# Kernel tuning notes

Measured on AMD Instinct MI355X. Metric: run time of the kernel, lower is better.

Reference implementation:

```python
import jax, jax.numpy as jnp
import numpy as np

B, N = 2, 131072          # batch, expanded node slots (divisible by flag_size)
FEAT = 69                 # org(3) + pos(3) + uids(63)
KERNELS = 128
FLAG_SIZE = 4             # 1 << dims, dims = 2
BINS = 16                 # 1 << flag_size


def _conv1d(x, w, b, stride=1, padding='SAME'):
    # keras Conv1D: x [B,N,Cin], w [K,Cin,Cout], relu activation
    y = jax.lax.conv_general_dilated(x, w, (stride,), padding,
                                     dimension_numbers=('NWC', 'WIO', 'NWC'))
    return jax.nn.relu(y + b)


def setup_inputs() -> dict:
    key = jax.random.key(0)
    ks = jax.random.split(key, 12)

    def g(k, shape):
        fan_in = int(np.prod(shape[:-1]))
        return (jax.random.normal(k, shape, jnp.float32) / np.sqrt(fan_in)).astype(jnp.float32)

    c_x = FEAT + KERNELS                 # 197 after each pre conv concat
    c_flags = 2 * FEAT + KERNELS         # 266 flags-head input
    c_sym = c_flags + FLAG_SIZE          # 270 symbols-branch input

    return {
        'inputs': jax.random.normal(ks[0], (B, N, FEAT), jnp.float32),
        'w_pre0': g(ks[1], (3, FEAT, KERNELS)),   'b_pre0': jnp.zeros((KERNELS,), jnp.float32),
        'w_pre1': g(ks[2], (3, c_x, KERNELS)),    'b_pre1': jnp.zeros((KERNELS,), jnp.float32),
        'w_flags': g(ks[3], (c_flags, FLAG_SIZE)), 'b_flags': jnp.zeros((FLAG_SIZE,), jnp.float32),
        'w_merge': g(ks[4], (FLAG_SIZE, c_sym, KERNELS)), 'b_merge': jnp.zeros((KERNELS,), jnp.float32),
        'w_post0': g(ks[5], (3, KERNELS, KERNELS)), 'b_post0': jnp.zeros((KERNELS,), jnp.float32),
        'w_post1': g(ks[6], (3, KERNELS, KERNELS)), 'b_post1': jnp.zeros((KERNELS,), jnp.float32),
        'w_post2': g(ks[7], (3, KERNELS, KERNELS)), 'b_post2': jnp.zeros((KERNELS,), jnp.float32),
        'w_post3': g(ks[8], (3, KERNELS, KERNELS)), 'b_post3': jnp.zeros((KERNELS,), jnp.float32),
        'w_sym': g(ks[9], (KERNELS, BINS)),        'b_sym': jnp.zeros((BINS,), jnp.float32),
    }


def _forward(inputs, w_pre0, b_pre0, w_pre1, b_pre1, w_flags, b_flags,
             w_merge, b_merge, w_post0, b_post0, w_post1, b_post1,
             w_post2, b_post2, w_post3, b_post3, w_sym, b_sym):
    # pos offsets = (3, 6); pos = inputs[..., 3:5] (2 columns)
    pos = inputs[..., 3:5]
    sort = jnp.argsort(pos, axis=-2)                       # [B, N, 2]
    # gather with batch_dims=1 along node axis
    X = jnp.take_along_axis(inputs, sort[..., 1:2], axis=1)   # sorted by pos col 1
    x0 = jax.lax.stop_gradient(X)                            # [B, N, 69]
    X = jnp.concatenate([x0, _conv1d(X, w_pre0, b_pre0)], axis=-1)  # [B, N, 197]
    X = jnp.concatenate([x0, _conv1d(X, w_pre1, b_pre1)], axis=-1)  # [B, N, 197]
    X = jnp.concatenate([X, jnp.take_along_axis(inputs, sort[..., 0:1], axis=1)], axis=-1)  # [B, N, 266]

    F = jax.nn.sigmoid(X @ w_flags + b_flags)               # [B, N, 4]

    S = jax.lax.stop_gradient(jnp.concatenate([F, X], axis=-1))     # [B, N, 270]
    S = _conv1d(S, w_merge, b_merge, stride=FLAG_SIZE, padding='VALID')  # [B, N/4, 128]
    for w, b in ((w_post0, b_post0), (w_post1, b_post1), (w_post2, b_post2), (w_post3, b_post3)):
        S = _conv1d(S, w, b)
    S = jax.nn.softmax(S @ w_sym + b_sym, axis=-1)          # [B, N/4, 16]

    Fd = (F[..., 0] - F[..., 1]).reshape(F.shape[0], -1, FLAG_SIZE)  # [B, N/4, 4]
    return jnp.concatenate([Fd, S], axis=-1)                # [B, N/4, 20]


def reference(inputs, w_pre0, b_pre0, w_pre1, b_pre1, w_flags, b_flags,
              w_merge, b_merge, w_post0, b_post0, w_post1, b_post1,
              w_post2, b_post2, w_post3, b_post3, w_sym, b_sym):
    return _forward(inputs, w_pre0, b_pre0, w_pre1, b_pre1, w_flags, b_flags,
                    w_merge, b_merge, w_post0, b_post0, w_post1, b_post1,
                    w_post2, b_post2, w_post3, b_post3, w_sym, b_sym)
```

## Files before the change

### kernel.cpp

```cpp
#include <hip/hip_runtime.h>
#include <hip/hip_bf16.h>
#include <math.h>

#define NPOS 131072
#define NF   69
#define NMRG 32768
#define TILE 2048
#define TPS  64
#define NSORT 4
#define EPT  16
#define XCW  288

typedef __attribute__((ext_vector_type(8))) short short8;
typedef __attribute__((ext_vector_type(4))) short s16x4;
typedef __bf16 bf16x8 __attribute__((ext_vector_type(8)));
typedef __attribute__((ext_vector_type(4))) float f32x4;

static __device__ inline bf16x8 as_bf16x8(short8 v){ union{short8 s; bf16x8 b;} u; u.s=v; return u.b; }
static __device__ inline short f2bf(float x){ __hip_bfloat16 h = __float2bfloat16(x); return *(short*)&h; }
static __device__ inline float bf2f(short s){ return __uint_as_float(((unsigned)(unsigned short)s)<<16); }

static __device__ inline void gld16(const short* g, short* l){
  __builtin_amdgcn_global_load_lds(
      (const __attribute__((address_space(1))) unsigned int*)g,
      (__attribute__((address_space(3))) unsigned int*)l, 16, 0, 0);
}

__global__ void k_make_keys(const float* __restrict__ inp, unsigned* __restrict__ kA,
                            unsigned* __restrict__ vA){
  unsigned t = blockIdx.x*256u + threadIdx.x;
  unsigned s = t >> 17, i = t & (NPOS-1u);
  unsigned b = s >> 1, ch = 3u + (s & 1u);
  float x = inp[((size_t)b*NPOS + i)*NF + ch];
  unsigned u = __float_as_uint(x);
  u = (u & 0x80000000u) ? ~u : (u | 0x80000000u);
  kA[t] = u; vA[t] = i;
}

__global__ __launch_bounds__(256) void k_hist(const unsigned* __restrict__ src,
                                              unsigned* __restrict__ hist, int shift){
  __shared__ unsigned h[256];
  int tid = threadIdx.x;
  h[tid] = 0u; __syncthreads();
  int s = blockIdx.x / TPS, tile = blockIdx.x % TPS;
  const unsigned* ks = src + (size_t)s*NPOS + (size_t)tile*TILE;
  for (int r = 0; r < TILE/256; ++r){
    unsigned d = (ks[r*256 + tid] >> shift) & 255u;
    atomicAdd(&h[d], 1u);
  }
  __syncthreads();
  hist[s*16384 + tid*TPS + tile] = h[tid];
}

__global__ __launch_bounds__(256) void k_scan(unsigned* __restrict__ hist){
  __shared__ unsigned tot[256];
  int tid = threadIdx.x; int s = blockIdx.x;
  unsigned* g = hist + s*16384;
  unsigned sum = 0;
  for (int q = 0; q < TPS; ++q) sum += g[tid*TPS + q];
  tot[tid] = sum;
  __syncthreads();
  if (tid == 0){
    unsigned run = 0;
    for (int t = 0; t < 256; ++t){ unsigned tmp = tot[t]; tot[t] = run; run += tmp; }
  }
  __syncthreads();
  unsigned run = tot[tid];
  for (int q = 0; q < TPS; ++q){ unsigned tmp = g[tid*TPS+q]; g[tid*TPS+q] = run; run += tmp; }
}

__global__ __launch_bounds__(128) void k_scatter(const unsigned* __restrict__ srcK,
    const unsigned* __restrict__ srcV, unsigned* __restrict__ dstK, unsigned* __restrict__ dstV,
    const unsigned* __restrict__ off, int shift){
  __shared__ unsigned short cnt[256*128];
  int tid = threadIdx.x;
  unsigned* cz = (unsigned*)cnt;
  for (int idx = tid; idx < 256*128/2; idx += 128) cz[idx] = 0u;
  __syncthreads();
  int s = blockIdx.x / TPS, tile = blockIdx.x % TPS;
  const unsigned* ks = srcK + (size_t)s*NPOS + (size_t)tile*TILE;
  const unsigned* vs = srcV + (size_t)s*NPOS + (size_t)tile*TILE;
  unsigned k8[EPT], v8[EPT];
  #pragma unroll
  for (int r = 0; r < EPT; ++r){
    k8[r] = ks[tid*EPT + r];
    v8[r] = vs[tid*EPT + r];
    unsigned d = (k8[r] >> shift) & 255u;
    cnt[d*128 + tid]++;
  }
  __syncthreads();
  for (int dd = 0; dd < 2; ++dd){
    int d = tid + dd*128;
    unsigned run = 0;
    for (int t = 0; t < 128; ++t){ unsigned tmp = cnt[d*128 + t]; cnt[d*128 + t] = (unsigned short)run; run += tmp; }
  }
  __syncthreads();
  const unsigned* ob = off + s*16384;
  #pragma unroll
  for (int r = 0; r < EPT; ++r){
    unsigned d = (k8[r] >> shift) & 255u;
    unsigned rk = cnt[d*128 + tid];
    cnt[d*128 + tid] = (unsigned short)(rk + 1u);
    unsigned pos = ob[d*TPS + tile] + rk;
    dstK[(size_t)s*NPOS + pos] = k8[r];
    dstV[(size_t)s*NPOS + pos] = v8[r];
  }
}

__global__ __launch_bounds__(256) void k_cvt(const float* __restrict__ inp,
                                             short* __restrict__ inpb, int b){
  int t = blockIdx.x*256 + threadIdx.x;
  int i = t/9, q = t - i*9;
  const float* sp = inp + ((size_t)b*NPOS + i)*NF + q*8;
  short o[8];
  #pragma unroll
  for (int e = 0; e < 8; ++e){
    int c = q*8 + e;
    o[e] = (c < NF) ? f2bf(sp[e]) : (short)0;
  }
  *(short8*)(inpb + (size_t)i*72 + q*8) = *(short8*)o;
}

__global__ __launch_bounds__(256) void k_gath2(const short* __restrict__ inpb,
    const unsigned* __restrict__ P1, const unsigned* __restrict__ P0,
    short* __restrict__ XA, short* __restrict__ Xcat){
  int t = blockIdx.x*256 + threadIdx.x;
  int i = t/18, u = t - i*18;
  int p = u/9, q = u - p*9;
  if (p){
    short8 v = *(const short8*)(inpb + (size_t)P1[i]*72 + q*8);
    *(short8*)(XA + (size_t)i*224 + 128 + q*8) = v;
    s16x4 lo = {v[0],v[1],v[2],v[3]}, hi = {v[4],v[5],v[6],v[7]};
    *(s16x4*)(Xcat + (size_t)i*XCW + 132 + q*8) = lo;
    *(s16x4*)(Xcat + (size_t)i*XCW + 136 + q*8) = hi;
  } else {
    short8 v = *(const short8*)(inpb + (size_t)P0[i]*72 + q*8);
    *(short8*)(Xcat + (size_t)i*XCW + 208 + q*8) = v;
    if (q == 8){
      s16x4 z4 = {0,0,0,0};
      *(s16x4*)(Xcat + (size_t)i*XCW + 204) = z4;
      short8 z8 = {0,0,0,0,0,0,0,0};
      *(short8*)(Xcat + (size_t)i*XCW + 280) = z8;
    }
  }
}

__global__ void k_prepB(const float* __restrict__ w, short* __restrict__ out,
                        int KC, int NQ, int mode, int total){
  int t = blockIdx.x*256 + threadIdx.x;
  if (t >= total) return;
  int lane = t & 63, ni = (t>>6) & 1, ksub = (t>>7) & 1;
  int rest = t >> 8;
  int q = rest % NQ;
  int wv = rest / NQ;
  int tap = q / KC, cc = q - tap*KC;
  int nn = wv*32 + ni*16 + (lane & 15);
  int chb = cc*64 + ksub*32 + ((lane >> 4) & 3)*8;
  short o[8];
  #pragma unroll
  for (int e = 0; e < 8; ++e){
    int ch = chb + e;
    float val = 0.f;
    if (mode == 0){ if (ch < 69)  val = w[((size_t)tap*69  + ch)*128 + nn]; }
    else if (mode == 1){
      if (ch < 128)      val = w[((size_t)tap*197 + 69 + ch)*128 + nn];
      else if (ch < 197) val = w[((size_t)tap*197 + ch - 128)*128 + nn];
    }
    else if (mode == 2){ if (ch < 128) val = w[((size_t)tap*128 + ch)*128 + nn]; }
    else {
      int tm = ch / XCW, cm = ch - tm*XCW;
      int orig = -1;
      if (cm < 128)                     orig = 73 + cm;
      else if (cm < 201)                orig = cm - 128;
      else if (cm >= 208 && cm < 277)   orig = cm - 7;
      if (orig >= 0) val = w[((size_t)tm*270 + orig)*128 + nn];
    }
    o[e] = f2bf(val);
  }
  *(short8*)(out + (size_t)t*8) = *(short8*)o;
}

__global__ void k_prepWf(const float* __restrict__ wf, float* __restrict__ out){
  int t = blockIdx.x*256 + threadIdx.x;
  if (t >= XCW*4) return;
  int c = t >> 2, q = t & 3;
  float v = 0.f;
  if (c < 128)                  v = wf[(69 + c)*4 + q];
  else if (c >= 132 && c < 201) v = wf[(c - 132)*4 + q];
  else if (c >= 208 && c < 277) v = wf[(197 + c - 208)*4 + q];
  out[t] = v;
}

#define OSTR2 136

template<int CPAD, int MT>
__global__ __launch_bounds__(256) void k_conv3s(
    const short* __restrict__ src, int sstride, int coff, int cin,
    const short* __restrict__ wB, const float* __restrict__ bias,
    short* __restrict__ dst, int dstride, int n)
{
  constexpr int KC  = CPAD/64;
  constexpr int KH  = CPAD/2;
  constexpr int KC2 = KH/64;
  constexpr int SPH = 3*KC2*2;
  constexpr int NST = 2*SPH;
  constexpr int PF  = 4;
  constexpr int ASTR = KH + 8;
  constexpr int AG  = KH/8;
  constexpr int MI  = MT/16;
  constexpr size_t ABYTES = (size_t)(MT+2)*ASTR*2;
  constexpr size_t OBYTES = (size_t)MT*OSTR2*2;
  constexpr size_t LBYTES = (ABYTES > OBYTES) ? ABYTES : OBYTES;
  __shared__ __attribute__((aligned(16))) char LDS[LBYTES];
  short* A_s = (short*)LDS;
  short* OTs = (short*)LDS;
  int tid = threadIdx.x;
  int i0 = blockIdx.x*MT;
  int wv = tid >> 6, lane = tid & 63;
  int lm = lane & 15, lk = lane >> 4;

  const short* wBw = wB + (size_t)wv*(KC*6)*1024 + (size_t)lane*8;
  auto LB = [&](int ls, int ni){
    int h = ls / SPH, r1 = ls % SPH;
    int tp = r1 / (KC2*2), r2 = r1 % (KC2*2);
    int c = r2 >> 1, ksub = r2 & 1;
    int q = tp*KC + h*KC2 + c;
    return as_bf16x8(*(const short8*)(wBw + ((q*2 + ksub)*2 + ni)*512));
  };
  auto stageA = [&](int h){
    for (int idx = tid; idx < (MT+2)*AG; idx += 256){
      int r = idx / AG, g = idx - r*AG;
      int pos = i0 - 1 + r;
      int cb = h*KH + g*8;
      short8 v = {0,0,0,0,0,0,0,0};
      if (pos >= 0 && pos < n && cb < cin){
        const short* sp = src + (size_t)pos*sstride + coff + cb;
        if (cb + 8 <= cin) v = *(const short8*)sp;
        else { for (int j = 0; cb + j < cin; ++j) v[j] = sp[j]; }
      }
      *(short8*)(A_s + r*ASTR + g*8) = v;
    }
  };

  bf16x8 bq[PF][2];
  #pragma unroll
  for (int s = 0; s < PF; ++s){ bq[s][0] = LB(s,0); bq[s][1] = LB(s,1); }
  stageA(0);
  __syncthreads();

  f32x4 acc[MI][2] = {};
  #pragma unroll
  for (int ls = 0; ls < NST; ++ls){
    if (ls == SPH){
      __syncthreads();
      stageA(1);
      __syncthreads();
    }
    int slot = ls % PF;
    bf16x8 b0 = bq[slot][0], b1 = bq[slot][1];
    if (ls + PF < NST){ bq[slot][0] = LB(ls+PF,0); bq[slot][1] = LB(ls+PF,1); }
    int r1 = ls % SPH;
    int tp = r1 / (KC2*2), r2 = r1 % (KC2*2);
    int c = r2 >> 1, ksub = r2 & 1;
    bf16x8 a[MI];
    #pragma unroll
    for (int mi = 0; mi < MI; ++mi)
      a[mi] = as_bf16x8(*(const short8*)(A_s + (mi*16+lm+tp)*ASTR + c*64 + ksub*32 + lk*8));
    #pragma unroll
    for (int mi = 0; mi < MI; ++mi){
      acc[mi][0] = __builtin_amdgcn_mfma_f32_16x16x32_bf16(a[mi], b0, acc[mi][0], 0, 0, 0);
      acc[mi][1] = __builtin_amdgcn_mfma_f32_16x16x32_bf16(a[mi], b1, acc[mi][1], 0, 0, 0);
    }
  }
  __syncthreads();
  float b0s = bias[wv*32 + lm], b1s = bias[wv*32 + 16 + lm];
  #pragma unroll
  for (int mi = 0; mi < MI; ++mi)
    #pragma unroll
    for (int ni = 0; ni < 2; ++ni){
      float bb = ni ? b1s : b0s;
      #pragma unroll
      for (int r = 0; r < 4; ++r)
        OTs[(mi*16 + lk*4 + r)*OSTR2 + wv*32 + ni*16 + lm] = f2bf(fmaxf(acc[mi][ni][r] + bb, 0.f));
    }
  __syncthreads();
  {
    constexpr int CPT = (MT*128/8)/256;
    int unit0 = tid*CPT;
    int r = unit0 >> 4, uq = unit0 & 15;
    const short* row = OTs + r*OSTR2 + uq*8;
    short* dp = dst + (size_t)(i0 + r)*dstride + uq*8;
    #pragma unroll
    for (int j = 0; j < CPT; ++j)
      *(short8*)(dp + j*8) = *(const short8*)(row + j*8);
  }
}

__global__ __launch_bounds__(256) void k_mergem4(const short* __restrict__ Xf,
    const short* __restrict__ wB, const float* __restrict__ bias, short* __restrict__ dst)
{
  constexpr int NS = 4*XCW/64;
  constexpr size_t ABYTES = 2*2048*2;
  constexpr size_t OBYTES = (size_t)32*OSTR2*2;
  constexpr size_t LBYTES = (ABYTES > OBYTES) ? ABYTES : OBYTES;
  __shared__ __attribute__((aligned(16))) char LDS[LBYTES];
  short* A_s = (short*)LDS;
  short* OTs = (short*)LDS;
  int tid = threadIdx.x;
  int j0 = blockIdx.x*32;
  int wv = tid >> 6, lane = tid & 63;
  int lm = lane & 15, lk = lane >> 4;
  auto stageA = [&](int s){
    int r = tid >> 3, kv = tid & 7;
    const short* gp = Xf + (size_t)(j0 + r)*(4*XCW) + s*64 + ((kv ^ (r&7))*8);
    gld16(gp, A_s + (s&1)*2048 + tid*8);
  };
  const short* wBl = wB + (size_t)wv*NS*2048 + (size_t)lane*8;
  auto LB = [&](int s, int ks, int ni){
    return as_bf16x8(*(const short8*)(wBl + ((size_t)(s*2 + ks)*2 + ni)*512));
  };
  bf16x8 c00 = LB(0,0,0), c01 = LB(0,0,1), c10 = LB(0,1,0), c11 = LB(0,1,1);
  stageA(0);
  __syncthreads();
  f32x4 acc[2][2] = {};
  for (int s = 0; s < NS; ++s){
    bf16x8 n00, n01, n10, n11;
    if (s < NS-1){
      n00 = LB(s+1,0,0); n01 = LB(s+1,0,1); n10 = LB(s+1,1,0); n11 = LB(s+1,1,1);
      stageA(s+1);
    }
    const short* Ab = A_s + (s&1)*2048;
    bf16x8 a[2];
    #pragma unroll
    for (int mi = 0; mi < 2; ++mi){
      int r = mi*16 + lm;
      a[mi] = as_bf16x8(*(const short8*)(Ab + r*64 + ((lk ^ (r&7))*8)));
    }
    #pragma unroll
    for (int mi = 0; mi < 2; ++mi){
      acc[mi][0] = __builtin_amdgcn_mfma_f32_16x16x32_bf16(a[mi], c00, acc[mi][0], 0, 0, 0);
      acc[mi][1] = __builtin_amdgcn_mfma_f32_16x16x32_bf16(a[mi], c01, acc[mi][1], 0, 0, 0);
    }
    #pragma unroll
    for (int mi = 0; mi < 2; ++mi){
      int r = mi*16 + lm;
      a[mi] = as_bf16x8(*(const short8*)(Ab + r*64 + (((4+lk) ^ (r&7))*8)));
    }
    #pragma unroll
    for (int mi = 0; mi < 2; ++mi){
      acc[mi][0] = __builtin_amdgcn_mfma_f32_16x16x32_bf16(a[mi], c10, acc[mi][0], 0, 0, 0);
      acc[mi][1] = __builtin_amdgcn_mfma_f32_16x16x32_bf16(a[mi], c11, acc[mi][1], 0, 0, 0);
    }
    __syncthreads();
    c00 = n00; c01 = n01; c10 = n10; c11 = n11;
  }
  float b0 = bias[wv*32 + lm], b1 = bias[wv*32 + 16 + lm];
  #pragma unroll
  for (int mi = 0; mi < 2; ++mi)
    #pragma unroll
    for (int ni = 0; ni < 2; ++ni){
      float bb = ni ? b1 : b0;
      #pragma unroll
      for (int r = 0; r < 4; ++r)
        OTs[(mi*16 + lk*4 + r)*OSTR2 + wv*32 + ni*16 + lm] = f2bf(fmaxf(acc[mi][ni][r] + bb, 0.f));
    }
  __syncthreads();
  {
    int unit0 = tid*2;
    int r = unit0 >> 4, uq = unit0 & 15;
    const short* row = OTs + r*OSTR2 + uq*8;
    short* dp = dst + (size_t)(j0 + r)*128 + uq*8;
    #pragma unroll
    for (int j = 0; j < 2; ++j)
      *(short8*)(dp + j*8) = *(const short8*)(row + j*8);
  }
}

__global__ __launch_bounds__(256) void k_flags2(short* __restrict__ Xcat,
    const float* __restrict__ Wf2, const float* __restrict__ bf, float* __restrict__ F){
  size_t i = (size_t)blockIdx.x*256 + threadIdx.x;
  const short* x = Xcat + i*XCW;
  float a0 = bf[0], a1 = bf[1], a2 = bf[2], a3 = bf[3];
  for (int g = 0; g < XCW/8; ++g){
    short8 x8 = *(const short8*)(x + g*8);
    #pragma unroll
    for (int e = 0; e < 8; ++e){
      float xv = bf2f(x8[e]);
      const float* w = Wf2 + (g*8+e)*4;
      a0 = fmaf(xv,w[0],a0); a1 = fmaf(xv,w[1],a1); a2 = fmaf(xv,w[2],a2); a3 = fmaf(xv,w[3],a3);
    }
  }
  float f0 = 1.f/(1.f+expf(-a0)), f1 = 1.f/(1.f+expf(-a1));
  float f2 = 1.f/(1.f+expf(-a2)), f3 = 1.f/(1.f+expf(-a3));
  float* f = F + i*4;
  f[0]=f0; f[1]=f1; f[2]=f2; f[3]=f3;
  short* xc = Xcat + i*XCW + 128;
  xc[0]=f2bf(f0); xc[1]=f2bf(f1); xc[2]=f2bf(f2); xc[3]=f2bf(f3);
}

__global__ __launch_bounds__(256) void k_out(const short* __restrict__ S,
    const float* __restrict__ F, const float* __restrict__ Ws, const float* __restrict__ bs,
    float* __restrict__ out, int b){
  size_t j = (size_t)blockIdx.x*256 + threadIdx.x;
  float l[16];
  #pragma unroll
  for (int t = 0; t < 16; ++t) l[t] = bs[t];
  const short* s = S + j*128;
  for (int g = 0; g < 16; ++g){
    short8 x8 = *(const short8*)(s + g*8);
    #pragma unroll
    for (int e = 0; e < 8; ++e){
      float x = bf2f(x8[e]);
      const float* w = Ws + (g*8+e)*16;
      #pragma unroll
      for (int t = 0; t < 16; ++t) l[t] = fmaf(x, w[t], l[t]);
    }
  }
  float m = l[0];
  #pragma unroll
  for (int t = 1; t < 16; ++t) m = fmaxf(m, l[t]);
  float sum = 0.f;
  #pragma unroll
  for (int t = 0; t < 16; ++t){ l[t] = expf(l[t]-m); sum += l[t]; }
  float inv = 1.f/sum;
  float* o = out + ((size_t)b*NMRG + j)*20;
  #pragma unroll
  for (int k = 0; k < 4; ++k){
    size_t r = (size_t)(4*j + k)*4;
    o[k] = F[r] - F[r+1];
  }
  #pragma unroll
  for (int t = 0; t < 16; ++t) o[4+t] = l[t]*inv;
}

extern "C" void kernel_launch(void* const* d_in, const int* in_sizes, int n_in,
                              void* d_out, int out_size, void* d_ws, size_t ws_size,
                              hipStream_t stream){
  const float* inp     = (const float*)d_in[0];
  const float* w_pre0  = (const float*)d_in[1];
  const float* b_pre0  = (const float*)d_in[2];
  const float* w_pre1  = (const float*)d_in[3];
  const float* b_pre1  = (const float*)d_in[4];
  const float* w_flags = (const float*)d_in[5];
  const float* b_flags = (const float*)d_in[6];
  const float* w_merge = (const float*)d_in[7];
  const float* b_merge = (const float*)d_in[8];
  const float* w_post[4] = {(const float*)d_in[9], (const float*)d_in[11],
                            (const float*)d_in[13], (const float*)d_in[15]};
  const float* b_post[4] = {(const float*)d_in[10], (const float*)d_in[12],
                            (const float*)d_in[14], (const float*)d_in[16]};
  const float* w_sym   = (const float*)d_in[17];
  const float* b_sym   = (const float*)d_in[18];
  float* outp = (float*)d_out;

  char* p = (char*)d_ws;
  unsigned* kA = (unsigned*)p; p += (size_t)NSORT*NPOS*4;
  unsigned* vA = (unsigned*)p; p += (size_t)NSORT*NPOS*4;
  unsigned* kB = (unsigned*)p; p += (size_t)NSORT*NPOS*4;
  unsigned* vB = (unsigned*)p; p += (size_t)NSORT*NPOS*4;
  unsigned* hist = (unsigned*)p; p += (size_t)NSORT*16384*4;
  short* inpb = (short*)p; p += (size_t)NPOS*72*2;
  short* XA   = (short*)p; p += (size_t)NPOS*224*2;
  short* Xcat = (short*)p; p += (size_t)NPOS*XCW*2;
  float* Fbuf = (float*)p; p += (size_t)NPOS*4*4;
  short* M0   = (short*)p; p += (size_t)NMRG*128*2;
  short* M1   = (short*)p; p += (size_t)NMRG*128*2;
  short* wb0  = (short*)p; p += (size_t)3*2*8192*2;
  short* wb1  = (short*)p; p += (size_t)3*4*8192*2;
  short* wbq0 = (short*)p; p += (size_t)3*2*8192*2;
  short* wbq1 = (short*)p; p += (size_t)3*2*8192*2;
  short* wbq2 = (short*)p; p += (size_t)3*2*8192*2;
  short* wbq3 = (short*)p; p += (size_t)3*2*8192*2;
  short* wbm  = (short*)p; p += (size_t)18*8192*2;
  float* wf2  = (float*)p; p += (size_t)XCW*4*4;
  if ((size_t)(p - (char*)d_ws) > ws_size) return;
  short* wbq[4] = {wbq0, wbq1, wbq2, wbq3};

  k_prepB<<<(6144 +255)/256, 256, 0, stream>>>(w_pre0, wb0, 2, 6, 0, 6144);
  k_prepB<<<(12288+255)/256, 256, 0, stream>>>(w_pre1, wb1, 4, 12, 1, 12288);
  for (int i = 0; i < 4; ++i)
    k_prepB<<<(6144+255)/256, 256, 0, stream>>>(w_post[i], wbq[i], 2, 6, 2, 6144);
  k_prepB<<<(18432+255)/256, 256, 0, stream>>>(w_merge, wbm, 18, 18, 3, 18432);
  k_prepWf<<<(XCW*4+255)/256, 256, 0, stream>>>(w_flags, wf2);

  k_make_keys<<<NSORT*NPOS/256, 256, 0, stream>>>(inp, kA, vA);
  unsigned *sk = kA, *sv = vA, *dk = kB, *dv = vB;
  for (int pass = 0; pass < 4; ++pass){
    int shift = pass*8;
    k_hist<<<NSORT*TPS, 256, 0, stream>>>(sk, hist, shift);
    k_scan<<<NSORT, 256, 0, stream>>>(hist);
    k_scatter<<<NSORT*TPS, 128, 0, stream>>>(sk, sv, dk, dv, hist, shift);
    unsigned* t;
    t = sk; sk = dk; dk = t;
    t = sv; sv = dv; dv = t;
  }
  for (int b = 0; b < 2; ++b){
    const unsigned* P0 = sv + (size_t)(b*2+0)*NPOS;
    const unsigned* P1 = sv + (size_t)(b*2+1)*NPOS;
    k_cvt<<<NPOS*9/256, 256, 0, stream>>>(inp, inpb, b);
    k_gath2<<<NPOS*18/256, 256, 0, stream>>>(inpb, P1, P0, XA, Xcat);
    k_conv3s<128,64><<<NPOS/64, 256, 0, stream>>>(XA, 224, 128, 69,  wb0, b_pre0, XA,   224, NPOS);
    k_conv3s<256,64><<<NPOS/64, 256, 0, stream>>>(XA, 224, 0,   197, wb1, b_pre1, Xcat, XCW, NPOS);
    k_flags2<<<NPOS/256, 256, 0, stream>>>(Xcat, wf2, b_flags, Fbuf);
    k_mergem4<<<NMRG/32, 256, 0, stream>>>(Xcat, wbm, b_merge, M0);
    k_conv3s<128,32><<<NMRG/32, 256, 0, stream>>>(M0, 128, 0, 128, wbq[0], b_post[0], M1, 128, NMRG);
    k_conv3s<128,32><<<NMRG/32, 256, 0, stream>>>(M1, 128, 0, 128, wbq[1], b_post[1], M0, 128, NMRG);
    k_conv3s<128,32><<<NMRG/32, 256, 0, stream>>>(M0, 128, 0, 128, wbq[2], b_post[2], M1, 128, NMRG);
    k_conv3s<128,32><<<NMRG/32, 256, 0, stream>>>(M1, 128, 0, 128, wbq[3], b_post[3], M0, 128, NMRG);
    k_out<<<NMRG/256, 256, 0, stream>>>(M0, Fbuf, w_sym, b_sym, outp, b);
  }
}
```

Baseline: 591.2 us.

## Fuse flags head and output softmax into conv kernels, merge weight prep

Merges all weight-preparation launches into one kernel. It fuses the flags sigmoid head into the epilogue of the second pre-conv, reading the just-written Xcat rows back from global memory after a barrier. It also fuses the symbol projection, softmax and flag-difference output into the last post conv, working from the LDS tile so M0 is never written. This removes several kernel launches and a full re-read of the Xcat and final activation buffers, at the cost of extra epilogue work and register pressure in the conv kernels.

```diff
diff --git a/kernel.cpp b/kernel.cpp
--- a/kernel.cpp
+++ b/kernel.cpp
@@ -145,10 +145,8 @@
   }
 }
 
-__global__ void k_prepB(const float* __restrict__ w, short* __restrict__ out,
-                        int KC, int NQ, int mode, int total){
-  int t = blockIdx.x*256 + threadIdx.x;
-  if (t >= total) return;
+static __device__ inline void prep_one(const float* __restrict__ w, short* __restrict__ out,
+                                       int t, int KC, int NQ, int mode){
   int lane = t & 63, ni = (t>>6) & 1, ksub = (t>>7) & 1;
   int rest = t >> 8;
   int q = rest % NQ;
@@ -180,24 +178,41 @@
   *(short8*)(out + (size_t)t*8) = *(short8*)o;
 }
 
-__global__ void k_prepWf(const float* __restrict__ wf, float* __restrict__ out){
+__global__ __launch_bounds__(256) void k_prepAll(
+    const float* __restrict__ w_pre0, const float* __restrict__ w_pre1,
+    const float* __restrict__ q0w, const float* __restrict__ q1w,
+    const float* __restrict__ q2w, const float* __restrict__ q3w,
+    const float* __restrict__ w_merge, const float* __restrict__ w_flags,
+    short* o0, short* o1, short* oq0, short* oq1, short* oq2, short* oq3,
+    short* om, float* owf){
   int t = blockIdx.x*256 + threadIdx.x;
-  if (t >= XCW*4) return;
-  int c = t >> 2, q = t & 3;
-  float v = 0.f;
-  if (c < 128)                  v = wf[(69 + c)*4 + q];
-  else if (c >= 132 && c < 201) v = wf[(c - 132)*4 + q];
-  else if (c >= 208 && c < 277) v = wf[(197 + c - 208)*4 + q];
-  out[t] = v;
+  if (t < 6144)        prep_one(w_pre0, o0,  t,        2,  6,  0);
+  else if (t < 18432)  prep_one(w_pre1, o1,  t-6144,   4,  12, 1);
+  else if (t < 24576)  prep_one(q0w,    oq0, t-18432,  2,  6,  2);
+  else if (t < 30720)  prep_one(q1w,    oq1, t-24576,  2,  6,  2);
+  else if (t < 36864)  prep_one(q2w,    oq2, t-30720,  2,  6,  2);
+  else if (t < 43008)  prep_one(q3w,    oq3, t-36864,  2,  6,  2);
+  else if (t < 61440)  prep_one(w_merge,om,  t-43008,  18, 18, 3);
+  else if (t < 62592){
+    int t2 = t - 61440;
+    int c = t2 >> 2, q = t2 & 3;
+    float v = 0.f;
+    if (c < 128)                  v = w_flags[(69 + c)*4 + q];
+    else if (c >= 132 && c < 201) v = w_flags[(c - 132)*4 + q];
+    else if (c >= 208 && c < 277) v = w_flags[(197 + c - 208)*4 + q];
+    owf[t2] = v;
+  }
 }
 
 #define OSTR2 136
 
-template<int CPAD, int MT>
+template<int CPAD, int MT, int FUSE>
 __global__ __launch_bounds__(256) void k_conv3s(
     const short* __restrict__ src, int sstride, int coff, int cin,
     const short* __restrict__ wB, const float* __restrict__ bias,
-    short* __restrict__ dst, int dstride, int n)
+    short* __restrict__ dst, int dstride, int n,
+    const float* __restrict__ ex1, const float* __restrict__ ex2,
+    float* __restrict__ ex3, const float* __restrict__ ex4)
 {
   constexpr int KC  = CPAD/64;
   constexpr int KH  = CPAD/2;
@@ -284,7 +299,8 @@
         OTs[(mi*16 + lk*4 + r)*OSTR2 + wv*32 + ni*16 + lm] = f2bf(fmaxf(acc[mi][ni][r] + bb, 0.f));
     }
   __syncthreads();
-  {
+
+  if constexpr (FUSE != 2){
     constexpr int CPT = (MT*128/8)/256;
     int unit0 = tid*CPT;
     int r = unit0 >> 4, uq = unit0 & 15;
@@ -293,6 +309,81 @@
     #pragma unroll
     for (int j = 0; j < CPT; ++j)
       *(short8*)(dp + j*8) = *(const short8*)(row + j*8);
+  }
+
+  if constexpr (FUSE == 1){
+    __syncthreads();
+    int row = tid >> 2, part = tid & 3;
+    const short* xr = dst + (size_t)(i0 + row)*dstride;
+    float a0 = 0.f, a1 = 0.f, a2 = 0.f, a3 = 0.f;
+    #pragma unroll
+    for (int g = 0; g < 9; ++g){
+      int ch = part*72 + g*8;
+      short8 x8 = *(const short8*)(xr + ch);
+      #pragma unroll
+      for (int e = 0; e < 8; ++e){
+        float xv = bf2f(x8[e]);
+        const float* w = ex1 + (ch + e)*4;
+        a0 = fmaf(xv,w[0],a0); a1 = fmaf(xv,w[1],a1);
+        a2 = fmaf(xv,w[2],a2); a3 = fmaf(xv,w[3],a3);
+      }
+    }
+    #pragma unroll
+    for (int m = 1; m < 4; m <<= 1){
+      a0 += __shfl_xor(a0, m); a1 += __shfl_xor(a1, m);
+      a2 += __shfl_xor(a2, m); a3 += __shfl_xor(a3, m);
+    }
+    if (part == 0){
+      float f0 = 1.f/(1.f+expf(-(a0 + ex2[0])));
+      float f1 = 1.f/(1.f+expf(-(a1 + ex2[1])));
+      float f2 = 1.f/(1.f+expf(-(a2 + ex2[2])));
+      float f3 = 1.f/(1.f+expf(-(a3 + ex2[3])));
+      float* fp = ex3 + (size_t)(i0 + row)*4;
+      fp[0]=f0; fp[1]=f1; fp[2]=f2; fp[3]=f3;
+      short* xc = dst + (size_t)(i0 + row)*dstride + 128;
+      xc[0]=f2bf(f0); xc[1]=f2bf(f1); xc[2]=f2bf(f2); xc[3]=f2bf(f3);
+    }
+  }
+
+  if constexpr (FUSE == 2){
+    int row = tid >> 3, part = tid & 7;
+    const short* srow = OTs + row*OSTR2 + part*16;
+    float l[16];
+    #pragma unroll
+    for (int t2 = 0; t2 < 16; ++t2) l[t2] = (part == 0) ? ex2[t2] : 0.f;
+    #pragma unroll
+    for (int g = 0; g < 2; ++g){
+      short8 x8 = *(const short8*)(srow + g*8);
+      #pragma unroll
+      for (int e = 0; e < 8; ++e){
+        float x = bf2f(x8[e]);
+        const float* w = ex1 + (part*16 + g*8 + e)*16;
+        #pragma unroll
+        for (int t2 = 0; t2 < 16; ++t2) l[t2] = fmaf(x, w[t2], l[t2]);
+      }
+    }
+    #pragma unroll
+    for (int m = 1; m < 8; m <<= 1)
+      #pragma unroll
+      for (int t2 = 0; t2 < 16; ++t2) l[t2] += __shfl_xor(l[t2], m);
+    if (part == 0){
+      float mx = l[0];
+      #pragma unroll
+      for (int t2 = 1; t2 < 16; ++t2) mx = fmaxf(mx, l[t2]);
+      float sum = 0.f;
+      #pragma unroll
+      for (int t2 = 0; t2 < 16; ++t2){ l[t2] = expf(l[t2]-mx); sum += l[t2]; }
+      float inv = 1.f/sum;
+      size_t j = (size_t)(i0 + row);
+      float* o = ex3 + j*20;
+      #pragma unroll
+      for (int k2 = 0; k2 < 4; ++k2){
+        size_t r4 = (size_t)(4*j + k2)*4;
+        o[k2] = ex4[r4] - ex4[r4+1];
+      }
+      #pragma unroll
+      for (int t2 = 0; t2 < 16; ++t2) o[4+t2] = l[t2]*inv;
+    }
   }
 }
 
@@ -376,63 +467,6 @@
   }
 }
 
-__global__ __launch_bounds__(256) void k_flags2(short* __restrict__ Xcat,
-    const float* __restrict__ Wf2, const float* __restrict__ bf, float* __restrict__ F){
-  size_t i = (size_t)blockIdx.x*256 + threadIdx.x;
-  const short* x = Xcat + i*XCW;
-  float a0 = bf[0], a1 = bf[1], a2 = bf[2], a3 = bf[3];
-  for (int g = 0; g < XCW/8; ++g){
-    short8 x8 = *(const short8*)(x + g*8);
-    #pragma unroll
-    for (int e = 0; e < 8; ++e){
-      float xv = bf2f(x8[e]);
-      const float* w = Wf2 + (g*8+e)*4;
-      a0 = fmaf(xv,w[0],a0); a1 = fmaf(xv,w[1],a1); a2 = fmaf(xv,w[2],a2); a3 = fmaf(xv,w[3],a3);
-    }
-  }
-  float f0 = 1.f/(1.f+expf(-a0)), f1 = 1.f/(1.f+expf(-a1));
-  float f2 = 1.f/(1.f+expf(-a2)), f3 = 1.f/(1.f+expf(-a3));
-  float* f = F + i*4;
-  f[0]=f0; f[1]=f1; f[2]=f2; f[3]=f3;
-  short* xc = Xcat + i*XCW + 128;
-  xc[0]=f2bf(f0); xc[1]=f2bf(f1); xc[2]=f2bf(f2); xc[3]=f2bf(f3);
-}
-
-__global__ __launch_bounds__(256) void k_out(const short* __restrict__ S,
-    const float* __restrict__ F, const float* __restrict__ Ws, const float* __restrict__ bs,
-    float* __restrict__ out, int b){
-  size_t j = (size_t)blockIdx.x*256 + threadIdx.x;
-  float l[16];
-  #pragma unroll
-  for (int t = 0; t < 16; ++t) l[t] = bs[t];
-  const short* s = S + j*128;
-  for (int g = 0; g < 16; ++g){
-    short8 x8 = *(const short8*)(s + g*8);
-    #pragma unroll
-    for (int e = 0; e < 8; ++e){
-      float x = bf2f(x8[e]);
-      const float* w = Ws + (g*8+e)*16;
-      #pragma unroll
-      for (int t = 0; t < 16; ++t) l[t] = fmaf(x, w[t], l[t]);
-    }
-  }
-  float m = l[0];
-  #pragma unroll
-  for (int t = 1; t < 16; ++t) m = fmaxf(m, l[t]);
-  float sum = 0.f;
-  #pragma unroll
-  for (int t = 0; t < 16; ++t){ l[t] = expf(l[t]-m); sum += l[t]; }
-  float inv = 1.f/sum;
-  float* o = out + ((size_t)b*NMRG + j)*20;
-  #pragma unroll
-  for (int k = 0; k < 4; ++k){
-    size_t r = (size_t)(4*j + k)*4;
-    o[k] = F[r] - F[r+1];
-  }
-  #pragma unroll
-  for (int t = 0; t < 16; ++t) o[4+t] = l[t]*inv;
-}
-
 extern "C" void kernel_launch(void* const* d_in, const int* in_sizes, int n_in,
                               void* d_out, int out_size, void* d_ws, size_t ws_size,
                               hipStream_t stream){
@@ -476,12 +510,9 @@
   if ((size_t)(p - (char*)d_ws) > ws_size) return;
   short* wbq[4] = {wbq0, wbq1, wbq2, wbq3};
 
-  k_prepB<<<(6144 +255)/256, 256, 0, stream>>>(w_pre0, wb0, 2, 6, 0, 6144);
-  k_prepB<<<(12288+255)/256, 256, 0, stream>>>(w_pre1, wb1, 4, 12, 1, 12288);
-  for (int i = 0; i < 4; ++i)
-    k_prepB<<<(6144+255)/256, 256, 0, stream>>>(w_post[i], wbq[i], 2, 6, 2, 6144);
-  k_prepB<<<(18432+255)/256, 256, 0, stream>>>(w_merge, wbm, 18, 18, 3, 18432);
-  k_prepWf<<<(XCW*4+255)/256, 256, 0, stream>>>(w_flags, wf2);
+  k_prepAll<<<(62592+255)/256, 256, 0, stream>>>(
+      w_pre0, w_pre1, w_post[0], w_post[1], w_post[2], w_post[3], w_merge, w_flags,
+      wb0, wb1, wbq0, wbq1, wbq2, wbq3, wbm, wf2);
 
   k_make_keys<<<NSORT*NPOS/256, 256, 0, stream>>>(inp, kA, vA);
   unsigned *sk = kA, *sv = vA, *dk = kB, *dv = vB;
@@ -499,14 +530,18 @@
     const unsigned* P1 = sv + (size_t)(b*2+1)*NPOS;
     k_cvt<<<NPOS*9/256, 256, 0, stream>>>(inp, inpb, b);
     k_gath2<<<NPOS*18/256, 256, 0, stream>>>(inpb, P1, P0, XA, Xcat);
-    k_conv3s<128,64><<<NPOS/64, 256, 0, stream>>>(XA, 224, 128, 69,  wb0, b_pre0, XA,   224, NPOS);
-    k_conv3s<256,64><<<NPOS/64, 256, 0, stream>>>(XA, 224, 0,   197, wb1, b_pre1, Xcat, XCW, NPOS);
-    k_flags2<<<NPOS/256, 256, 0, stream>>>(Xcat, wf2, b_flags, Fbuf);
+    k_conv3s<128,64,0><<<NPOS/64, 256, 0, stream>>>(XA, 224, 128, 69, wb0, b_pre0, XA, 224, NPOS,
+                                                    nullptr, nullptr, nullptr, nullptr);
+    k_conv3s<256,64,1><<<NPOS/64, 256, 0, stream>>>(XA, 224, 0, 197, wb1, b_pre1, Xcat, XCW, NPOS,
+                                                    wf2, b_flags, Fbuf, nullptr);
     k_mergem4<<<NMRG/32, 256, 0, stream>>>(Xcat, wbm, b_merge, M0);
-    k_conv3s<128,32><<<NMRG/32, 256, 0, stream>>>(M0, 128, 0, 128, wbq[0], b_post[0], M1, 128, NMRG);
-    k_conv3s<128,32><<<NMRG/32, 256, 0, stream>>>(M1, 128, 0, 128, wbq[1], b_post[1], M0, 128, NMRG);
-    k_conv3s<128,32><<<NMRG/32, 256, 0, stream>>>(M0, 128, 0, 128, wbq[2], b_post[2], M1, 128, NMRG);
-    k_conv3s<128,32><<<NMRG/32, 256, 0, stream>>>(M1, 128, 0, 128, wbq[3], b_post[3], M0, 128, NMRG);
-    k_out<<<NMRG/256, 256, 0, stream>>>(M0, Fbuf, w_sym, b_sym, outp, b);
-  }
-}
+    k_conv3s<128,32,0><<<NMRG/32, 256, 0, stream>>>(M0, 128, 0, 128, wbq[0], b_post[0], M1, 128, NMRG,
+                                                    nullptr, nullptr, nullptr, nullptr);
+    k_conv3s<128,32,0><<<NMRG/32, 256, 0, stream>>>(M1, 128, 0, 128, wbq[1], b_post[1], M0, 128, NMRG,
+                                                    nullptr, nullptr, nullptr, nullptr);
+    k_conv3s<128,32,0><<<NMRG/32, 256, 0, stream>>>(M0, 128, 0, 128, wbq[2], b_post[2], M1, 128, NMRG,
+                                                    nullptr, nullptr, nullptr, nullptr);
+    k_conv3s<128,32,2><<<NMRG/32, 256, 0, stream>>>(M1, 128, 0, 128, wbq[3], b_post[3], M0, 128, NMRG,
+                                                    w_sym, b_sym, outp + (size_t)b*NMRG*20, Fbuf);
+  }
+}
```

New measurement: 679.0 us. 1.15x slower.

## Split conv and merge warp tiles 2x2 over rows and output channels

Applied to the files above, without the earlier changes.

Changes the per-wave work split in the conv3 and merge MFMA kernels. Before, each of the four waves owned 32 output channels across all rows. Now waves form a 2x2 grid: each owns half the rows and 64 channels. This halves each wave's LDS A-fragment reads but doubles its weight-register loads from global and the number of prefetched B fragments it holds. That raises register pressure and global weight traffic per wave, which may cost occupancy.

```diff
diff --git a/kernel.cpp b/kernel.cpp
--- a/kernel.cpp
+++ b/kernel.cpp
@@ -207,7 +207,7 @@
   constexpr int PF  = 4;
   constexpr int ASTR = KH + 8;
   constexpr int AG  = KH/8;
-  constexpr int MI  = MT/16;
+  constexpr int MI2 = MT/32;
   constexpr size_t ABYTES = (size_t)(MT+2)*ASTR*2;
   constexpr size_t OBYTES = (size_t)MT*OSTR2*2;
   constexpr size_t LBYTES = (ABYTES > OBYTES) ? ABYTES : OBYTES;
@@ -217,15 +217,18 @@
   int tid = threadIdx.x;
   int i0 = blockIdx.x*MT;
   int wv = tid >> 6, lane = tid & 63;
+  int wm = wv >> 1, wn = wv & 1;
   int lm = lane & 15, lk = lane >> 4;
 
-  const short* wBw = wB + (size_t)wv*(KC*6)*1024 + (size_t)lane*8;
-  auto LB = [&](int ls, int ni){
+  const short* wBw = wB + (size_t)lane*8;
+  auto LB = [&](int ls, int j){
     int h = ls / SPH, r1 = ls % SPH;
     int tp = r1 / (KC2*2), r2 = r1 % (KC2*2);
     int c = r2 >> 1, ksub = r2 & 1;
     int q = tp*KC + h*KC2 + c;
-    return as_bf16x8(*(const short8*)(wBw + ((q*2 + ksub)*2 + ni)*512));
+    int g32 = wn*2 + (j >> 1);
+    return as_bf16x8(*(const short8*)(wBw + (size_t)g32*(KC*6)*1024
+                                          + ((q*2 + ksub)*2 + (j & 1))*512));
   };
   auto stageA = [&](int h){
     for (int idx = tid; idx < (MT+2)*AG; idx += 256){
@@ -242,13 +245,15 @@
     }
   };
 
-  bf16x8 bq[PF][2];
-  #pragma unroll
-  for (int s = 0; s < PF; ++s){ bq[s][0] = LB(s,0); bq[s][1] = LB(s,1); }
+  bf16x8 bq[PF][4];
+  #pragma unroll
+  for (int s = 0; s < PF; ++s)
+    #pragma unroll
+    for (int j = 0; j < 4; ++j) bq[s][j] = LB(s, j);
   stageA(0);
   __syncthreads();
 
-  f32x4 acc[MI][2] = {};
+  f32x4 acc[MI2][4] = {};
   #pragma unroll
   for (int ls = 0; ls < NST; ++ls){
     if (ls == SPH){
@@ -257,31 +262,39 @@
       __syncthreads();
     }
     int slot = ls % PF;
-    bf16x8 b0 = bq[slot][0], b1 = bq[slot][1];
-    if (ls + PF < NST){ bq[slot][0] = LB(ls+PF,0); bq[slot][1] = LB(ls+PF,1); }
+    bf16x8 b0 = bq[slot][0], b1 = bq[slot][1], b2 = bq[slot][2], b3 = bq[slot][3];
+    if (ls + PF < NST){
+      #pragma unroll
+      for (int j = 0; j < 4; ++j) bq[slot][j] = LB(ls+PF, j);
+    }
     int r1 = ls % SPH;
     int tp = r1 / (KC2*2), r2 = r1 % (KC2*2);
     int c = r2 >> 1, ksub = r2 & 1;
-    bf16x8 a[MI];
-    #pragma unroll
-    for (int mi = 0; mi < MI; ++mi)
-      a[mi] = as_bf16x8(*(const short8*)(A_s + (mi*16+lm+tp)*ASTR + c*64 + ksub*32 + lk*8));
-    #pragma unroll
-    for (int mi = 0; mi < MI; ++mi){
+    bf16x8 a[MI2];
+    #pragma unroll
+    for (int mi = 0; mi < MI2; ++mi)
+      a[mi] = as_bf16x8(*(const short8*)(A_s + (wm*(MT/2) + mi*16 + lm + tp)*ASTR
+                                             + c*64 + ksub*32 + lk*8));
+    #pragma unroll
+    for (int mi = 0; mi < MI2; ++mi){
       acc[mi][0] = __builtin_amdgcn_mfma_f32_16x16x32_bf16(a[mi], b0, acc[mi][0], 0, 0, 0);
       acc[mi][1] = __builtin_amdgcn_mfma_f32_16x16x32_bf16(a[mi], b1, acc[mi][1], 0, 0, 0);
-    }
-  }
-  __syncthreads();
-  float b0s = bias[wv*32 + lm], b1s = bias[wv*32 + 16 + lm];
-  #pragma unroll
-  for (int mi = 0; mi < MI; ++mi)
-    #pragma unroll
-    for (int ni = 0; ni < 2; ++ni){
-      float bb = ni ? b1s : b0s;
+      acc[mi][2] = __builtin_amdgcn_mfma_f32_16x16x32_bf16(a[mi], b2, acc[mi][2], 0, 0, 0);
+      acc[mi][3] = __builtin_amdgcn_mfma_f32_16x16x32_bf16(a[mi], b3, acc[mi][3], 0, 0, 0);
+    }
+  }
+  __syncthreads();
+  float bs[4];
+  #pragma unroll
+  for (int j = 0; j < 4; ++j) bs[j] = bias[wn*64 + j*16 + lm];
+  #pragma unroll
+  for (int mi = 0; mi < MI2; ++mi)
+    #pragma unroll
+    for (int j = 0; j < 4; ++j){
       #pragma unroll
       for (int r = 0; r < 4; ++r)
-        OTs[(mi*16 + lk*4 + r)*OSTR2 + wv*32 + ni*16 + lm] = f2bf(fmaxf(acc[mi][ni][r] + bb, 0.f));
+        OTs[(wm*(MT/2) + mi*16 + lk*4 + r)*OSTR2 + wn*64 + j*16 + lm]
+            = f2bf(fmaxf(acc[mi][j][r] + bs[j], 0.f));
     }
   __syncthreads();
   {
@@ -309,61 +322,56 @@
   int tid = threadIdx.x;
   int j0 = blockIdx.x*32;
   int wv = tid >> 6, lane = tid & 63;
+  int wm = wv >> 1, wn = wv & 1;
   int lm = lane & 15, lk = lane >> 4;
   auto stageA = [&](int s){
     int r = tid >> 3, kv = tid & 7;
     const short* gp = Xf + (size_t)(j0 + r)*(4*XCW) + s*64 + ((kv ^ (r&7))*8);
     gld16(gp, A_s + (s&1)*2048 + tid*8);
   };
-  const short* wBl = wB + (size_t)wv*NS*2048 + (size_t)lane*8;
-  auto LB = [&](int s, int ks, int ni){
-    return as_bf16x8(*(const short8*)(wBl + ((size_t)(s*2 + ks)*2 + ni)*512));
+  const short* wBl = wB + (size_t)lane*8;
+  auto LB = [&](int s, int ks, int j){
+    int g32 = wn*2 + (j >> 1);
+    return as_bf16x8(*(const short8*)(wBl + (size_t)g32*NS*2048
+                                          + ((size_t)((s*2 + ks)*2 + (j & 1)))*512));
   };
-  bf16x8 c00 = LB(0,0,0), c01 = LB(0,0,1), c10 = LB(0,1,0), c11 = LB(0,1,1);
+  bf16x8 c0[4], c1[4];
+  #pragma unroll
+  for (int j = 0; j < 4; ++j){ c0[j] = LB(0,0,j); c1[j] = LB(0,1,j); }
   stageA(0);
   __syncthreads();
-  f32x4 acc[2][2] = {};
+  f32x4 acc[4] = {};
   for (int s = 0; s < NS; ++s){
-    bf16x8 n00, n01, n10, n11;
+    bf16x8 n0[4], n1[4];
     if (s < NS-1){
-      n00 = LB(s+1,0,0); n01 = LB(s+1,0,1); n10 = LB(s+1,1,0); n11 = LB(s+1,1,1);
+      #pragma unroll
+      for (int j = 0; j < 4; ++j){ n0[j] = LB(s+1,0,j); n1[j] = LB(s+1,1,j); }
       stageA(s+1);
     }
     const short* Ab = A_s + (s&1)*2048;
-    bf16x8 a[2];
-    #pragma unroll
-    for (int mi = 0; mi < 2; ++mi){
-      int r = mi*16 + lm;
-      a[mi] = as_bf16x8(*(const short8*)(Ab + r*64 + ((lk ^ (r&7))*8)));
-    }
-    #pragma unroll
-    for (int mi = 0; mi < 2; ++mi){
-      acc[mi][0] = __builtin_amdgcn_mfma_f32_16x16x32_bf16(a[mi], c00, acc[mi][0], 0, 0, 0);
-      acc[mi][1] = __builtin_amdgcn_mfma_f32_16x16x32_bf16(a[mi], c01, acc[mi][1], 0, 0, 0);
-    }
-    #pragma unroll
-    for (int mi = 0; mi < 2; ++mi){
-      int r = mi*16 + lm;
-      a[mi] = as_bf16x8(*(const short8*)(Ab + r*64 + (((4+lk) ^ (r&7))*8)));
-    }
-    #pragma unroll
-    for (int mi = 0; mi < 2; ++mi){
-      acc[mi][0] = __builtin_amdgcn_mfma_f32_16x16x32_bf16(a[mi], c10, acc[mi][0], 0, 0, 0);
-      acc[mi][1] = __builtin_amdgcn_mfma_f32_16x16x32_bf16(a[mi], c11, acc[mi][1], 0, 0, 0);
-    }
+    int r = wm*16 + lm;
+    bf16x8 a0 = as_bf16x8(*(const short8*)(Ab + r*64 + ((lk ^ (r&7))*8)));
+    #pragma unroll
+    for (int j = 0; j < 4; ++j)
+      acc[j] = __builtin_amdgcn_mfma_f32_16x16x32_bf16(a0, c0[j], acc[j], 0, 0, 0);
+    bf16x8 a1 = as_bf16x8(*(const short8*)(Ab + r*64 + (((4+lk) ^ (r&7))*8)));
+    #pragma unroll
+    for (int j = 0; j < 4; ++j)
+      acc[j] = __builtin_amdgcn_mfma_f32_16x16x32_bf16(a1, c1[j], acc[j], 0, 0, 0);
     __syncthreads();
-    c00 = n00; c01 = n01; c10 = n10; c11 = n11;
-  }
-  float b0 = bias[wv*32 + lm], b1 = bias[wv*32 + 16 + lm];
-  #pragma unroll
-  for (int mi = 0; mi < 2; ++mi)
-    #pragma unroll
-    for (int ni = 0; ni < 2; ++ni){
-      float bb = ni ? b1 : b0;
-      #pragma unroll
-      for (int r = 0; r < 4; ++r)
-        OTs[(mi*16 + lk*4 + r)*OSTR2 + wv*32 + ni*16 + lm] = f2bf(fmaxf(acc[mi][ni][r] + bb, 0.f));
-    }
+    #pragma unroll
+    for (int j = 0; j < 4; ++j){ c0[j] = n0[j]; c1[j] = n1[j]; }
+  }
+  float bs[4];
+  #pragma unroll
+  for (int j = 0; j < 4; ++j) bs[j] = bias[wn*64 + j*16 + lm];
+  #pragma unroll
+  for (int j = 0; j < 4; ++j){
+    #pragma unroll
+    for (int r = 0; r < 4; ++r)
+      OTs[(wm*16 + lk*4 + r)*OSTR2 + wn*64 + j*16 + lm]
+          = f2bf(fmaxf(acc[j][r] + bs[j], 0.f));
+  }
   __syncthreads();
   {
     int unit0 = tid*2;
```

After: 662.0 us. 1.12x slower.
